# Kernel tuning notes

Measured on AMD Instinct MI355X. Metric: run time of the kernel, lower is better.

## Reference

```python
import jax, jax.numpy as jnp
import numpy as np

SIGMA = 1.0
TWOPI = 2.0 * np.pi
NORM_FACTOR = 90.0474


def _realspace_potential(q, r, u):
    # q: [n], r: [n,3], u: [n,3]  (n_q = 1)
    n = r.shape[0]
    dt = r.dtype
    q2 = q[:, None]            # [n, 1]
    u3 = u[:, None, :]         # [n, 1, 3]

    a = 1.0 / (SIGMA * np.sqrt(2.0))
    c = 2.0 * a / np.sqrt(np.pi)

    mask_off = ~jnp.eye(n, dtype=bool)
    m = mask_off.astype(dt)
    trilf = jnp.tril(jnp.ones((n, n), dt), -1)  # j < i pairs

    r_ij = r[None, :, :] - r[:, None, :]                       # [n,n,3]
    rsq = jnp.sum(r_ij * r_ij, axis=-1)                        # [n,n]
    rnorm = jnp.sqrt(jnp.where(mask_off, rsq, 1.0))            # safe on diagonal
    rinv = m / rnorm
    rinv2 = rinv * rinv
    rinv3 = rinv2 * rinv
    erf = m * jax.lax.erf(a * rnorm)
    gauss = m * jnp.exp(-(a * rnorm) ** 2)

    # charge-charge
    f_qq = erf * rinv
    pot = jnp.sum(trilf[:, :, None] * (q2[None, :, :] * q2[:, None, :] * f_qq[:, :, None])) / TWOPI

    # charge-dipole
    s1 = erf * rinv3 - c * gauss * rinv2
    f_qu = -s1[:, :, None] * r_ij                              # [n,n,3]
    ui_T = jnp.einsum('iqc,ijc->ijq', u3, f_qu)
    T_uj = jnp.einsum('ijc,jqc->ijq', f_qu, u3)
    pot_qu_ij = ui_T * q2[None, :, :] - q2[:, None, :] * T_uj
    pot = pot + jnp.sum(trilf[:, :, None] * pot_qu_ij) / TWOPI

    # dipole-dipole
    # 4 a^3 / sqrt(pi) = 2 a^2 * c ; 4 a / sqrt(pi) = 2 c
    s2 = s1 - 2.0 * a * a * c * gauss - c * gauss * rinv2 + 2.0 * erf * rinv3
    rhat = r_ij * rinv[..., None]
    outer = rhat[:, :, :, None] * rhat[:, :, None, :]          # [n,n,3,3]
    I3 = jnp.eye(3, dtype=dt)
    f_uu = s2[:, :, None, None] * outer - s1[:, :, None, None] * I3[None, None]
    pot = pot - 0.5 * jnp.einsum('iqc,ijcd,jqd->', u3, f_uu, u3) / TWOPI

    # remove_self_interaction=True -> no self term added
    return pot * NORM_FACTOR


def setup_inputs() -> dict:
    key = jax.random.key(0)
    k1, k2, k3 = jax.random.split(key, 3)
    n = 2048
    q = jax.random.normal(k1, (n,), dtype=jnp.float32)
    r = jax.random.uniform(k2, (n, 3), dtype=jnp.float32) * 20.0  # positions in a 20 A box
    u = jax.random.normal(k3, (n, 3), dtype=jnp.float32) * 0.1    # dipoles
    return {"q": q, "r": r, "u": u}


def reference(q, r, u):
    return _realspace_potential(q, r, u)
```

## Files before the change

### kernel.cpp

```cpp
#include <hip/hip_runtime.h>
#include <math.h>

#ifndef M_PI
#define M_PI 3.14159265358979323846
#endif

constexpr int N_ATOMS = 2048;
constexpr int BLOCK   = 256;
constexpr int JT      = 32;
constexpr int GRID_I  = N_ATOMS / BLOCK;
constexpr int GRID_J  = N_ATOMS / JT;
constexpr int NPART   = GRID_I * GRID_J;

__global__ __launch_bounds__(BLOCK) void ewald_pairs(
    const float* __restrict__ q, const float* __restrict__ r,
    const float* __restrict__ u, float* __restrict__ partial)
{
    __shared__ float sq[JT], srx[JT], sry[JT], srz[JT], sux[JT], suy[JT], suz[JT];
    __shared__ float swave[BLOCK / 64];

    const int tid = threadIdx.x;
    const int i   = blockIdx.x * BLOCK + tid;
    const int j0  = blockIdx.y * JT;

    if (tid < JT) {
        const int j = j0 + tid;
        sq[tid]  = q[j];
        srx[tid] = r[3 * j + 0]; sry[tid] = r[3 * j + 1]; srz[tid] = r[3 * j + 2];
        sux[tid] = u[3 * j + 0]; suy[tid] = u[3 * j + 1]; suz[tid] = u[3 * j + 2];
    }
    __syncthreads();

    const float qi  = q[i];
    const float rix = r[3 * i + 0], riy = r[3 * i + 1], riz = r[3 * i + 2];
    const float uix = u[3 * i + 0], uiy = u[3 * i + 1], uiz = u[3 * i + 2];

    const float A = 0.70710678118654752f;
    const float C = 0.79788456080286536f;

    float acc = 0.0f;

#pragma unroll 8
    for (int jj = 0; jj < JT; ++jj) {
        const int   j  = j0 + jj;
        const float dx = srx[jj] - rix;
        const float dy = sry[jj] - riy;
        const float dz = srz[jj] - riz;
        float rsq = dx * dx + dy * dy + dz * dz;
        const bool diag = (j == i);
        rsq = diag ? 1.0f : rsq;

        const float rinv  = __builtin_amdgcn_rsqf(rsq);
        const float rn    = rsq * rinv;
        const float erfv  = erff(A * rn);
        const float g     = __expf(-0.5f * rsq);
        const float rinv2 = rinv * rinv;
        const float er3   = erfv * rinv2 * rinv;
        const float cg2   = C * g * rinv2;
        const float s1    = er3 - cg2;
        const float s2    = 3.0f * er3 - 2.0f * cg2 - C * g;

        const float ujx = sux[jj], ujy = suy[jj], ujz = suz[jj];
        const float uid  = uix * dx + uiy * dy + uiz * dz;
        const float ujd  = ujx * dx + ujy * dy + ujz * dz;
        const float uiuj = uix * ujx + uiy * ujy + uiz * ujz;
        const float qj   = sq[jj];

        float t = qi * qj * erfv * rinv
                - s1 * (uid * qj - qi * ujd)
                - (s2 * rinv2 * uid * ujd - s1 * uiuj);
        acc += diag ? 0.0f : t;
    }

    for (int off = 32; off > 0; off >>= 1)
        acc += __shfl_down(acc, off, 64);
    const int lane = tid & 63, wave = tid >> 6;
    if (lane == 0) swave[wave] = acc;
    __syncthreads();
    if (tid == 0) {
        float s = 0.0f;
        for (int w = 0; w < BLOCK / 64; ++w) s += swave[w];
        partial[blockIdx.y * gridDim.x + blockIdx.x] = s;
    }
}

__global__ __launch_bounds__(256) void ewald_reduce(
    const float* __restrict__ partial, float* __restrict__ out)
{
    __shared__ float swave[4];
    float v = 0.0f;
    for (int k = threadIdx.x; k < NPART; k += 256) v += partial[k];
    for (int off = 32; off > 0; off >>= 1)
        v += __shfl_down(v, off, 64);
    const int lane = threadIdx.x & 63, wave = threadIdx.x >> 6;
    if (lane == 0) swave[wave] = v;
    __syncthreads();
    if (threadIdx.x == 0) {
        const float SCALE = (float)(0.5 * 90.0474 / (2.0 * M_PI));
        out[0] = (swave[0] + swave[1] + swave[2] + swave[3]) * SCALE;
    }
}

extern "C" void kernel_launch(void* const* d_in, const int* in_sizes, int n_in,
                              void* d_out, int out_size, void* d_ws, size_t ws_size,
                              hipStream_t stream) {
    const float* q = (const float*)d_in[0];
    const float* r = (const float*)d_in[1];
    const float* u = (const float*)d_in[2];
    float* partial = (float*)d_ws;

    dim3 grid(GRID_I, GRID_J);
    ewald_pairs<<<grid, BLOCK, 0, stream>>>(q, r, u, partial);
    ewald_reduce<<<1, 256, 0, stream>>>(partial, (float*)d_out);
}
```

Baseline: 70.01 us.

## Exploit pair symmetry to compute only lower triangle and use polynomial erf

Computes only j<i pairs by skipping tiles above the diagonal and dropping the 0.5 factor, which roughly halves the pairwise work. It swaps erff for the Abramowitz-Stegun polynomial that reuses the existing Gaussian, and shrinks blocks to one 64-lane wave that loads j data straight from global memory instead of shared memory. The polynomial erf is less accurate, the diagonal tiles waste some lanes, and the skipped blocks still launch.

```diff
diff --git a/kernel.cpp b/kernel.cpp
--- a/kernel.cpp
+++ b/kernel.cpp
@@ -6,82 +6,78 @@
 #endif
 
 constexpr int N_ATOMS = 2048;
-constexpr int BLOCK   = 256;
+constexpr int BLOCK   = 64;
+constexpr int ICH     = 64;
 constexpr int JT      = 32;
-constexpr int GRID_I  = N_ATOMS / BLOCK;
-constexpr int GRID_J  = N_ATOMS / JT;
-constexpr int NPART   = GRID_I * GRID_J;
+constexpr int GI      = N_ATOMS / ICH;
+constexpr int GJ      = N_ATOMS / JT;
+constexpr int NPART   = GI * GJ;
 
 __global__ __launch_bounds__(BLOCK) void ewald_pairs(
     const float* __restrict__ q, const float* __restrict__ r,
     const float* __restrict__ u, float* __restrict__ partial)
 {
-    __shared__ float sq[JT], srx[JT], sry[JT], srz[JT], sux[JT], suy[JT], suz[JT];
-    __shared__ float swave[BLOCK / 64];
+    const int bi  = blockIdx.x, bj = blockIdx.y;
+    const int pid = bi * GJ + bj;
 
-    const int tid = threadIdx.x;
-    const int i   = blockIdx.x * BLOCK + tid;
-    const int j0  = blockIdx.y * JT;
+    if (bj > 2 * bi + 1) {
+        if (threadIdx.x == 0) partial[pid] = 0.0f;
+        return;
+    }
 
-    if (tid < JT) {
-        const int j = j0 + tid;
-        sq[tid]  = q[j];
-        srx[tid] = r[3 * j + 0]; sry[tid] = r[3 * j + 1]; srz[tid] = r[3 * j + 2];
-        sux[tid] = u[3 * j + 0]; suy[tid] = u[3 * j + 1]; suz[tid] = u[3 * j + 2];
-    }
-    __syncthreads();
+    const int i  = bi * ICH + threadIdx.x;
+    const int j0 = bj * JT;
 
     const float qi  = q[i];
     const float rix = r[3 * i + 0], riy = r[3 * i + 1], riz = r[3 * i + 2];
     const float uix = u[3 * i + 0], uiy = u[3 * i + 1], uiz = u[3 * i + 2];
 
-    const float A = 0.70710678118654752f;
-    const float C = 0.79788456080286536f;
+    const float C  = 0.79788456080286536f;
+    const float PA = 0.23166036f;
+    const float A1 = 0.254829592f, A2 = -0.284496736f, A3 = 1.421413741f;
+    const float A4 = -1.453152027f, A5 = 1.061405429f;
 
     float acc = 0.0f;
 
 #pragma unroll 8
     for (int jj = 0; jj < JT; ++jj) {
-        const int   j  = j0 + jj;
-        const float dx = srx[jj] - rix;
-        const float dy = sry[jj] - riy;
-        const float dz = srz[jj] - riz;
-        float rsq = dx * dx + dy * dy + dz * dz;
-        const bool diag = (j == i);
-        rsq = diag ? 1.0f : rsq;
+        const int j = j0 + jj;
+        const float qj  = q[j];
+        const float rjx = r[3 * j + 0], rjy = r[3 * j + 1], rjz = r[3 * j + 2];
+        const float ujx = u[3 * j + 0], ujy = u[3 * j + 1], ujz = u[3 * j + 2];
 
-        const float rinv  = __builtin_amdgcn_rsqf(rsq);
-        const float rn    = rsq * rinv;
-        const float erfv  = erff(A * rn);
-        const float g     = __expf(-0.5f * rsq);
+        const float dx = rjx - rix, dy = rjy - riy, dz = rjz - riz;
+        const float rsq = dx * dx + dy * dy + dz * dz;
+
+        const float rinv = __builtin_amdgcn_rsqf(rsq);
+        const float rn   = rsq * rinv;
+        const float g    = __expf(-0.5f * rsq);
+
+        const float t5 = __builtin_amdgcn_rcpf(fmaf(PA, rn, 1.0f));
+        const float poly = t5 * fmaf(t5, fmaf(t5, fmaf(t5, fmaf(t5, A5, A4), A3), A2), A1);
+        const float erfv = 1.0f - poly * g;
+
         const float rinv2 = rinv * rinv;
         const float er3   = erfv * rinv2 * rinv;
-        const float cg2   = C * g * rinv2;
+        const float Cg    = C * g;
+        const float cg2   = Cg * rinv2;
         const float s1    = er3 - cg2;
-        const float s2    = 3.0f * er3 - 2.0f * cg2 - C * g;
+        const float s2    = fmaf(3.0f, er3, -2.0f * cg2) - Cg;
 
-        const float ujx = sux[jj], ujy = suy[jj], ujz = suz[jj];
         const float uid  = uix * dx + uiy * dy + uiz * dz;
         const float ujd  = ujx * dx + ujy * dy + ujz * dz;
         const float uiuj = uix * ujx + uiy * ujy + uiz * ujz;
-        const float qj   = sq[jj];
 
-        float t = qi * qj * erfv * rinv
-                - s1 * (uid * qj - qi * ujd)
-                - (s2 * rinv2 * uid * ujd - s1 * uiuj);
-        acc += diag ? 0.0f : t;
+        const float t = qi * qj * erfv * rinv
+                      - s1 * (uid * qj - qi * ujd)
+                      - (s2 * rinv2 * uid * ujd - s1 * uiuj);
+
+        acc += (j < i) ? t : 0.0f;
     }
 
     for (int off = 32; off > 0; off >>= 1)
         acc += __shfl_down(acc, off, 64);
-    const int lane = tid & 63, wave = tid >> 6;
-    if (lane == 0) swave[wave] = acc;
-    __syncthreads();
-    if (tid == 0) {
-        float s = 0.0f;
-        for (int w = 0; w < BLOCK / 64; ++w) s += swave[w];
-        partial[blockIdx.y * gridDim.x + blockIdx.x] = s;
-    }
+    if (threadIdx.x == 0) partial[pid] = acc;
 }
 
 __global__ __launch_bounds__(256) void ewald_reduce(
@@ -92,11 +88,10 @@
     for (int k = threadIdx.x; k < NPART; k += 256) v += partial[k];
     for (int off = 32; off > 0; off >>= 1)
         v += __shfl_down(v, off, 64);
-    const int lane = threadIdx.x & 63, wave = threadIdx.x >> 6;
-    if (lane == 0) swave[wave] = v;
+    if ((threadIdx.x & 63) == 0) swave[threadIdx.x >> 6] = v;
     __syncthreads();
     if (threadIdx.x == 0) {
-        const float SCALE = (float)(0.5 * 90.0474 / (2.0 * M_PI));
+        const float SCALE = (float)(90.0474 / (2.0 * M_PI));
         out[0] = (swave[0] + swave[1] + swave[2] + swave[3]) * SCALE;
     }
 }
@@ -109,7 +104,7 @@
     const float* u = (const float*)d_in[2];
     float* partial = (float*)d_ws;
 
-    dim3 grid(GRID_I, GRID_J);
+    dim3 grid(GI, GJ);
     ewald_pairs<<<grid, BLOCK, 0, stream>>>(q, r, u, partial);
     ewald_reduce<<<1, 256, 0, stream>>>(partial, (float*)d_out);
 }
```

Result: faster. 68.52 us (-2.1%).
